# Optimization experiments

Measured on AMD Instinct MI355X. Metric: run time of the kernel, lower is better.

Reference implementation:

```python
import jax, jax.numpy as jnp
import numpy as np

COMMITMENT_COST = 0.25


def setup_inputs() -> dict:
    key = jax.random.key(0)
    k1, k2 = jax.random.split(key)
    inputs = jax.random.normal(k1, (32, 1024, 256), dtype=jnp.float32)
    codebook = jax.random.normal(k2, (8192, 256), dtype=jnp.float32)
    return {"inputs": inputs, "codebook": codebook}


def reference(inputs, codebook):
    input_shape = inputs.shape
    D = codebook.shape[1]
    K = codebook.shape[0]
    flat = inputs.reshape(-1, D)                      # [N, D]
    N = flat.shape[0]

    distances = (
        jnp.sum(flat * flat, axis=1, keepdims=True)
        + jnp.sum(codebook * codebook, axis=1)
        - 2.0 * flat @ codebook.T
    )                                                  # [N, K]
    idx = jnp.argmin(distances, axis=1)               # [N]

    # gather (equivalent to one-hot @ codebook)
    quantized = jnp.take(codebook, idx, axis=0).reshape(input_shape)

    # straight-through estimator
    quantized_st = inputs + jax.lax.stop_gradient(quantized - inputs)

    e_latent_loss = jnp.mean((jax.lax.stop_gradient(quantized_st) - inputs) ** 2)
    q_latent_loss = jnp.mean((quantized - jax.lax.stop_gradient(inputs)) ** 2)
    commitment_loss = COMMITMENT_COST * e_latent_loss
    codebook_loss = q_latent_loss
    vq_loss = commitment_loss + codebook_loss

    # perplexity of codebook usage (avg one-hot probs)
    counts = jnp.zeros((K,), dtype=inputs.dtype).at[idx].add(1.0)
    avg_probs = counts / N
    perplexity = jnp.exp(-jnp.sum(avg_probs * jnp.log(avg_probs + 1e-10)))

    tokens = idx.reshape(input_shape[:-1])
    return quantized_st, tokens, vq_loss, commitment_loss, codebook_loss, perplexity
```

## Files before the change

### kernel.cpp

```cpp
#include <hip/hip_runtime.h>
#include <stdint.h>

typedef unsigned short u16;
typedef unsigned long long u64;

#define N_ROWS 32768
#define DIM 256
#define K_CODES 8192
#define TAU 0.3f

#define A_OFF     0ull
#define B_OFF     16777216ull
#define CN_OFF    20971520ull
#define PART1_OFF 21004288ull
#define PART2_OFF 22052864ull
#define IDX_OFF   22577152ull
#define HIST_OFF  22708224ull
#define CNT_OFF   22740992ull
#define FLAG_OFF  22741008ull
#define LOSS_OFF  22872080ull
#define CBT_OFF   23068672ull
#define GMIN2_OFF 31457280ull

#define OUT_Q 0
#define OUT_T 8388608
#define OUT_S 8421376

#define BM 128
#define BN 128
#define BK 64
#define JSPLIT 4
#define RSPLIT 4

#define PACK_INF ((((u64)0xFF800000u) << 32) | 0xFFFFFFFFull)

typedef _Float16 half8 __attribute__((ext_vector_type(8)));
typedef float floatx4 __attribute__((ext_vector_type(4)));

__device__ __forceinline__ void gload_lds16(const void* g, void* l) {
    __builtin_amdgcn_global_load_lds(
        (const __attribute__((address_space(1))) void*)g,
        (__attribute__((address_space(3))) void*)l,
        16, 0, 0);
}

__device__ __forceinline__ unsigned sortable(float v) {
    unsigned u = __float_as_uint(v);
    return (u & 0x80000000u) ? ~u : (u | 0x80000000u);
}
__device__ __forceinline__ float unsortable(unsigned u) {
    return (u & 0x80000000u) ? __uint_as_float(u & 0x7fffffffu) : __uint_as_float(~u);
}
__device__ __forceinline__ u64 shfl64x(u64 v, int m) {
    return ((u64)(unsigned)__shfl_xor((int)(v >> 32), m, 64) << 32) |
           (unsigned)__shfl_xor((int)(v & 0xffffffffu), m, 64);
}
__device__ __forceinline__ u64 u64min(u64 a, u64 b) { return a < b ? a : b; }
__device__ __forceinline__ u64 u64max(u64 a, u64 b) { return a > b ? a : b; }

__global__ void prep(const float* __restrict__ inp, const float* __restrict__ cb,
                     u16* __restrict__ A, u16* __restrict__ B, float* __restrict__ cn) {
    int g = blockIdx.x * 256 + threadIdx.x;
    int row = g >> 5;
    int kc = (g & 31) << 3;
    bool isA = row < N_ROWS;
    const float* src = isA ? inp + (size_t)row * DIM + kc
                           : cb + (size_t)(row - N_ROWS) * DIM + kc;
    u16* dst = isA ? A + (size_t)row * DIM + kc
                   : B + (size_t)(row - N_ROWS) * DIM + kc;
    float4 x0 = *(const float4*)(src);
    float4 x1 = *(const float4*)(src + 4);
    float xs[8] = {x0.x, x0.y, x0.z, x0.w, x1.x, x1.y, x1.z, x1.w};
    half8 hv;
    float s = 0.f;
#pragma unroll
    for (int i = 0; i < 8; ++i) {
        hv[i] = (_Float16)xs[i];
        s = fmaf(xs[i], xs[i], s);
    }
    *(half8*)(dst) = hv;
    if (!isA) {
#pragma unroll
        for (int m = 1; m <= 16; m <<= 1) s += __shfl_xor(s, m, 64);
        if ((g & 31) == 0) cn[row - N_ROWS] = s;
    }
}

__global__ void transpose_cb(const float* __restrict__ cb, float* __restrict__ cbT) {
    __shared__ float tile[64][65];
    const int tid = threadIdx.x;
    const int tj = blockIdx.x * 64;
    const int td = blockIdx.y * 64;
    const int c = (tid & 15) * 4;
    const int r0 = tid >> 4;
#pragma unroll
    for (int p = 0; p < 4; ++p) {
        int r = p * 16 + r0;
        float4 v = *(const float4*)(cb + (size_t)(tj + r) * DIM + td + c);
        tile[r][c] = v.x; tile[r][c + 1] = v.y; tile[r][c + 2] = v.z; tile[r][c + 3] = v.w;
    }
    __syncthreads();
#pragma unroll
    for (int p = 0; p < 4; ++p) {
        int rr = p * 16 + r0;
        float4 w = {tile[c][rr], tile[c + 1][rr], tile[c + 2][rr], tile[c + 3][rr]};
        *(float4*)(cbT + (size_t)(td + rr) * K_CODES + tj + c) = w;
    }
}

__launch_bounds__(256, 2)
__global__ void vq_pass1(const u16* __restrict__ A, const u16* __restrict__ B,
                         const float* __restrict__ cn,
                         u64* __restrict__ part1, float* __restrict__ part2) {
    __shared__ __align__(16) _Float16 lsA[BM * BK];
    __shared__ __align__(16) _Float16 lsB[BN * BK];
    __shared__ u64 t1buf[BM];
    __shared__ float t2buf[BM];

    const int tid = threadIdx.x;
    const int lane = tid & 63;
    const int w = tid >> 6;
    const int wm = w >> 1, wn = w & 1;
    const int l15 = lane & 15;
    const int quad = lane >> 4;
    const int xm = l15 & 7;
    const int rowBase = blockIdx.x * BM;
    const int jBase = blockIdx.y * (K_CODES / JSPLIT);

    float d1[16], d2[16];
    unsigned idxr[16];
#pragma unroll
    for (int i = 0; i < 16; ++i) {
        d1[i] = __builtin_inff(); d2[i] = __builtin_inff(); idxr[i] = 0xffffffffu;
    }

    const int str = tid >> 3;
    const int sk16 = tid & 7;

    for (int jc = 0; jc < (K_CODES / JSPLIT) / BN; ++jc) {
        const int colBase = jBase + jc * BN;
        floatx4 acc[4][4];
#pragma unroll
        for (int mi = 0; mi < 4; ++mi)
#pragma unroll
            for (int ni = 0; ni < 4; ++ni)
                acc[mi][ni] = (floatx4){0.f, 0.f, 0.f, 0.f};

#pragma unroll 1
        for (int kk = 0; kk < DIM; kk += BK) {
#pragma unroll
            for (int it = 0; it < 4; ++it) {
                int r = it * 32 + str;
                int cdat = sk16 ^ (r & 7);
                int ch = it * 256 + tid;
                gload_lds16(A + (size_t)(rowBase + r) * DIM + kk + cdat * 8,
                            (char*)lsA + ch * 16);
                gload_lds16(B + (size_t)(colBase + r) * DIM + kk + cdat * 8,
                            (char*)lsB + ch * 16);
            }
            __syncthreads();
#pragma unroll
            for (int s = 0; s < 2; ++s) {
                const int koff = ((s * 4 + quad) ^ xm) * 8;
                half8 af[4], bf[4];
#pragma unroll
                for (int mi = 0; mi < 4; ++mi)
                    af[mi] = *(const half8*)(lsA + (wm * 64 + mi * 16 + l15) * BK + koff);
#pragma unroll
                for (int ni = 0; ni < 4; ++ni)
                    bf[ni] = *(const half8*)(lsB + (wn * 64 + ni * 16 + l15) * BK + koff);
#pragma unroll
                for (int mi = 0; mi < 4; ++mi)
#pragma unroll
                    for (int ni = 0; ni < 4; ++ni)
                        acc[mi][ni] = __builtin_amdgcn_mfma_f32_16x16x32_f16(
                            af[mi], bf[ni], acc[mi][ni], 0, 0, 0);
            }
            __syncthreads();
        }

#pragma unroll
        for (int ni = 0; ni < 4; ++ni) {
            unsigned j = (unsigned)(colBase + wn * 64 + ni * 16 + l15);
            float cnj = cn[j];
#pragma unroll
            for (int mi = 0; mi < 4; ++mi) {
#pragma unroll
                for (int r = 0; r < 4; ++r) {
                    int tr = mi * 4 + r;
                    float val = fmaf(-2.0f, acc[mi][ni][r], cnj);
                    bool lt = val < d1[tr];
                    float sec = lt ? d1[tr] : val;
                    d2[tr] = fminf(d2[tr], sec);
                    d1[tr] = lt ? val : d1[tr];
                    idxr[tr] = lt ? j : idxr[tr];
                }
            }
        }
    }

    u64 m1[16];
#pragma unroll
    for (int tr = 0; tr < 16; ++tr)
        m1[tr] = ((u64)sortable(d1[tr]) << 32) | idxr[tr];
#pragma unroll
    for (int m = 1; m <= 8; m <<= 1)
#pragma unroll
        for (int tr = 0; tr < 16; ++tr) {
            u64 o1 = shfl64x(m1[tr], m);
            float o2 = __shfl_xor(d2[tr], m, 64);
            u64 n1 = u64min(m1[tr], o1);
            float big = unsortable((unsigned)(u64max(m1[tr], o1) >> 32));
            d2[tr] = fminf(big, fminf(d2[tr], o2));
            m1[tr] = n1;
        }

    if (wn == 0 && l15 == 0) {
#pragma unroll
        for (int tr = 0; tr < 16; ++tr) {
            int rl = wm * 64 + (tr >> 2) * 16 + quad * 4 + (tr & 3);
            t1buf[rl] = m1[tr]; t2buf[rl] = d2[tr];
        }
    }
    __syncthreads();
    if (wn == 1 && l15 == 0) {
#pragma unroll
        for (int tr = 0; tr < 16; ++tr) {
            int rl = wm * 64 + (tr >> 2) * 16 + quad * 4 + (tr & 3);
            u64 o1 = t1buf[rl];
            float o2 = t2buf[rl];
            u64 n1 = u64min(m1[tr], o1);
            float big = unsortable((unsigned)(u64max(m1[tr], o1) >> 32));
            float n2 = fminf(big, fminf(d2[tr], o2));
            size_t p = (size_t)(rowBase + rl) * JSPLIT + blockIdx.y;
            part1[p] = n1;
            part2[p] = n2;
        }
    }
}

__global__ void vq_merge(const u64* __restrict__ part1, const float* __restrict__ part2,
                         unsigned* __restrict__ idx32,
                         int* __restrict__ flaglist, int* __restrict__ cnt) {
    int row = blockIdx.x * 256 + threadIdx.x;
    u64 m1 = PACK_INF;
    float f2 = __builtin_inff();
#pragma unroll
    for (int y = 0; y < JSPLIT; ++y) {
        u64 p1 = part1[(size_t)row * JSPLIT + y];
        float p2 = part2[(size_t)row * JSPLIT + y];
        u64 n1 = u64min(m1, p1);
        float big = unsortable((unsigned)(u64max(m1, p1) >> 32));
        f2 = fminf(big, fminf(f2, p2));
        m1 = n1;
    }
    idx32[row] = (unsigned)(m1 & 0xffffffffu);
    float f1 = unsortable((unsigned)(m1 >> 32));
    if (f2 - f1 < TAU) {
        int p = atomicAdd(cnt, 1);
        flaglist[p] = row;
    }
}

__global__ void vq_recompute(const float* __restrict__ inp, const float* __restrict__ cbT,
                             const float* __restrict__ cn, const int* __restrict__ flaglist,
                             const int* __restrict__ cnt, u64* __restrict__ gmin2) {
    __shared__ float xsT[DIM][8];
    __shared__ u64 wred[8][8];
    const int tid = threadIdx.x;
    const int w = tid >> 6, lane = tid & 63;
    const int n = *cnt;
    const int base = blockIdx.x * 8;
    if (base >= n) return;

    {
        int li = base + w;
        int row = flaglist[li < n ? li : (n - 1)];
        float4 a = ((const float4*)(inp + (size_t)row * DIM))[lane];
        int d0 = lane * 4;
        xsT[d0 + 0][w] = a.x; xsT[d0 + 1][w] = a.y;
        xsT[d0 + 2][w] = a.z; xsT[d0 + 3][w] = a.w;
    }
    __syncthreads();

    const int cbase = blockIdx.y * (K_CODES / RSPLIT) + tid * 4;
    float4 acc[8];
#pragma unroll
    for (int r = 0; r < 8; ++r) acc[r] = (float4){0.f, 0.f, 0.f, 0.f};

    float4 cv = *(const float4*)(cbT + cbase);
#pragma unroll 4
    for (int d = 0; d < DIM - 1; ++d) {
        float4 nx = *(const float4*)(cbT + (size_t)(d + 1) * K_CODES + cbase);
        float4 xa = *(const float4*)&xsT[d][0];
        float4 xb = *(const float4*)&xsT[d][4];
        float xv[8] = {xa.x, xa.y, xa.z, xa.w, xb.x, xb.y, xb.z, xb.w};
#pragma unroll
        for (int r = 0; r < 8; ++r) {
            acc[r].x = fmaf(xv[r], cv.x, acc[r].x);
            acc[r].y = fmaf(xv[r], cv.y, acc[r].y);
            acc[r].z = fmaf(xv[r], cv.z, acc[r].z);
            acc[r].w = fmaf(xv[r], cv.w, acc[r].w);
        }
        cv = nx;
    }
    {
        const int d = DIM - 1;
        float4 xa = *(const float4*)&xsT[d][0];
        float4 xb = *(const float4*)&xsT[d][4];
        float xv[8] = {xa.x, xa.y, xa.z, xa.w, xb.x, xb.y, xb.z, xb.w};
#pragma unroll
        for (int r = 0; r < 8; ++r) {
            acc[r].x = fmaf(xv[r], cv.x, acc[r].x);
            acc[r].y = fmaf(xv[r], cv.y, acc[r].y);
            acc[r].z = fmaf(xv[r], cv.z, acc[r].z);
            acc[r].w = fmaf(xv[r], cv.w, acc[r].w);
        }
    }

    u64 best[8];
    float4 cn4 = *(const float4*)(cn + cbase);
#pragma unroll
    for (int r = 0; r < 8; ++r) {
        float d0 = cn4.x - 2.0f * acc[r].x;
        float d1 = cn4.y - 2.0f * acc[r].y;
        float d2 = cn4.z - 2.0f * acc[r].z;
        float d3 = cn4.w - 2.0f * acc[r].w;
        u64 b = ((u64)sortable(d0) << 32) | (unsigned)(cbase + 0);
        b = u64min(b, ((u64)sortable(d1) << 32) | (unsigned)(cbase + 1));
        b = u64min(b, ((u64)sortable(d2) << 32) | (unsigned)(cbase + 2));
        b = u64min(b, ((u64)sortable(d3) << 32) | (unsigned)(cbase + 3));
        best[r] = b;
    }

#pragma unroll
    for (int m = 1; m <= 32; m <<= 1)
#pragma unroll
        for (int r = 0; r < 8; ++r) best[r] = u64min(best[r], shfl64x(best[r], m));
    if (lane < 8) wred[w][lane] = best[lane];
    __syncthreads();
    if (tid < 8 && base + tid < n) {
        u64 b = wred[0][tid];
#pragma unroll
        for (int ww = 1; ww < 8; ++ww) b = u64min(b, wred[ww][tid]);
        atomicMin(&gmin2[flaglist[base + tid]], b);
    }
}

__global__ void vq_writeback(const u64* __restrict__ gmin2, const int* __restrict__ flaglist,
                             const int* __restrict__ cnt, unsigned* __restrict__ idx32) {
    int i = blockIdx.x * 256 + threadIdx.x;
    if (i < *cnt) {
        int row = flaglist[i];
        idx32[row] = (unsigned)(gmin2[row] & 0xffffffffull);
    }
}

__global__ void vq_gather(const float* __restrict__ inp, const float* __restrict__ cb,
                          const unsigned* __restrict__ idx32, float* __restrict__ out,
                          float* __restrict__ losspart, unsigned int* __restrict__ hist) {
    __shared__ float red[4];
    int w = threadIdx.x >> 6, lane = threadIdx.x & 63;
    int i = blockIdx.x * 4 + w;
    unsigned idx = idx32[i];
    float4 c = ((const float4*)(cb + (size_t)idx * DIM))[lane];
    float4 x = ((const float4*)(inp + (size_t)i * DIM))[lane];
    ((float4*)(out + OUT_Q))[(size_t)i * 64 + lane] = c;
    float dx = c.x - x.x, dy = c.y - x.y, dz = c.z - x.z, dw = c.w - x.w;
    float s = dx * dx + dy * dy + dz * dz + dw * dw;
#pragma unroll
    for (int m = 32; m; m >>= 1) s += __shfl_xor(s, m, 64);
    if (lane == 0) {
        out[OUT_T + i] = (float)idx;
        red[w] = s;
        atomicAdd(&hist[idx], 1u);
    }
    __syncthreads();
    if (threadIdx.x == 0)
        losspart[blockIdx.x] = red[0] + red[1] + red[2] + red[3];
}

__global__ void vq_finalize(const unsigned int* __restrict__ hist,
                            const float* __restrict__ losspart, float* __restrict__ out) {
    __shared__ float redp[256], redl[256];
    int tid = threadIdx.x;
    float sp = 0.f, sl = 0.f;
    for (int k = tid; k < K_CODES; k += 256) {
        float p = (float)hist[k] * (1.0f / (float)N_ROWS);
        sp += p * logf(p + 1e-10f);
        sl += losspart[k];
    }
    redp[tid] = sp; redl[tid] = sl;
    __syncthreads();
    for (int st = 128; st; st >>= 1) {
        if (tid < st) { redp[tid] += redp[tid + st]; redl[tid] += redl[tid + st]; }
        __syncthreads();
    }
    if (tid == 0) {
        float perp = expf(-redp[0]);
        float e = redl[0] / 8388608.0f;
        out[OUT_S + 0] = 1.25f * e;
        out[OUT_S + 1] = 0.25f * e;
        out[OUT_S + 2] = e;
        out[OUT_S + 3] = perp;
    }
}

extern "C" void kernel_launch(void* const* d_in, const int* in_sizes, int n_in,
                              void* d_out, int out_size, void* d_ws, size_t ws_size,
                              hipStream_t stream) {
    const float* inp = (const float*)d_in[0];
    const float* cb = (const float*)d_in[1];
    float* out = (float*)d_out;
    char* ws = (char*)d_ws;
    u16* A = (u16*)(ws + A_OFF);
    u16* B = (u16*)(ws + B_OFF);
    float* cn = (float*)(ws + CN_OFF);
    u64* part1 = (u64*)(ws + PART1_OFF);
    float* part2 = (float*)(ws + PART2_OFF);
    unsigned* idx32 = (unsigned*)(ws + IDX_OFF);
    unsigned int* hist = (unsigned int*)(ws + HIST_OFF);
    int* cnt = (int*)(ws + CNT_OFF);
    int* flaglist = (int*)(ws + FLAG_OFF);
    float* losspart = (float*)(ws + LOSS_OFF);
    float* cbT = (float*)(ws + CBT_OFF);
    u64* gmin2 = (u64*)(ws + GMIN2_OFF);

    hipMemsetAsync(hist, 0, K_CODES * 4 + 16, stream);
    hipMemsetAsync(gmin2, 0xFF, N_ROWS * 8, stream);

    prep<<<5120, 256, 0, stream>>>(inp, cb, A, B, cn);
    transpose_cb<<<dim3(K_CODES / 64, DIM / 64), 256, 0, stream>>>(cb, cbT);
    vq_pass1<<<dim3(N_ROWS / BM, JSPLIT), 256, 0, stream>>>(A, B, cn, part1, part2);
    vq_merge<<<N_ROWS / 256, 256, 0, stream>>>(part1, part2, idx32, flaglist, cnt);
    vq_recompute<<<dim3(N_ROWS / 8, RSPLIT), 512, 0, stream>>>(inp, cbT, cn, flaglist, cnt, gmin2);
    vq_writeback<<<N_ROWS / 256, 256, 0, stream>>>(gmin2, flaglist, cnt, idx32);
    vq_gather<<<N_ROWS / 4, 256, 0, stream>>>(inp, cb, idx32, out, losspart, hist);
    vq_finalize<<<1, 256, 0, stream>>>(hist, losspart, out);
}
```

Measured before the change: 403.2 us.

## Keep A tile in registers and double-buffer codebook tiles in pass1

Measured after the change: 410.8 us. No clear change (+1.9%).

```diff
diff --git a/kernel.cpp b/kernel.cpp
--- a/kernel.cpp
+++ b/kernel.cpp
@@ -27,9 +27,9 @@
 #define OUT_S 8421376
 
 #define BM 128
-#define BN 128
-#define BK 64
+#define BNT 64
 #define JSPLIT 4
+#define NJC ((K_CODES / JSPLIT) / BNT)
 #define RSPLIT 4
 
 #define PACK_INF ((((u64)0xFF800000u) << 32) | 0xFFFFFFFFull)
@@ -108,96 +108,106 @@
     }
 }
 
-__launch_bounds__(256, 2)
+#define STAGE_B(BUFP, JCV)                                                    \
+    {                                                                         \
+        const u16* bsrc = B + (size_t)(jBase + (JCV) * BNT) * DIM;            \
+        _Pragma("unroll")                                                     \
+        for (int r_ = 0; r_ < 4; ++r_) {                                      \
+            int idx_ = r_ * 512 + tid;                                        \
+            int col_ = idx_ >> 5;                                             \
+            int sc_ = idx_ & 31;                                              \
+            int csrc_ = (sc_ & 24) | ((sc_ & 7) ^ (col_ & 7));                \
+            gload_lds16(bsrc + (size_t)col_ * DIM + csrc_ * 8,                \
+                        (char*)(BUFP) + idx_ * 16);                           \
+        }                                                                     \
+    }
+
+#define TOP2(JT, CNV)                                                         \
+    {                                                                         \
+        unsigned jj = (unsigned)(jBase + (JT) * BNT + colLoc);                \
+        _Pragma("unroll")                                                     \
+        for (int mi_ = 0; mi_ < 4; ++mi_) {                                   \
+            _Pragma("unroll")                                                 \
+            for (int r_ = 0; r_ < 4; ++r_) {                                  \
+                int tr_ = mi_ * 4 + r_;                                       \
+                float val_ = fmaf(-2.0f, acc[mi_][r_], (CNV));                \
+                float nd2_ = __builtin_amdgcn_fmed3f(d1[tr_], d2[tr_], val_); \
+                bool lt_ = val_ < d1[tr_];                                    \
+                d1[tr_] = fminf(d1[tr_], val_);                               \
+                idxr[tr_] = lt_ ? jj : idxr[tr_];                             \
+                d2[tr_] = nd2_;                                               \
+            }                                                                 \
+        }                                                                     \
+    }
+
+__launch_bounds__(512, 2)
 __global__ void vq_pass1(const u16* __restrict__ A, const u16* __restrict__ B,
                          const float* __restrict__ cn,
                          u64* __restrict__ part1, float* __restrict__ part2) {
-    __shared__ __align__(16) _Float16 lsA[BM * BK];
-    __shared__ __align__(16) _Float16 lsB[BN * BK];
-    __shared__ u64 t1buf[BM];
-    __shared__ float t2buf[BM];
+    __shared__ __align__(16) _Float16 lsB[2][BNT * DIM];
 
     const int tid = threadIdx.x;
     const int lane = tid & 63;
     const int w = tid >> 6;
-    const int wm = w >> 1, wn = w & 1;
+    const int wm = w >> 2;
+    const int wn = w & 3;
     const int l15 = lane & 15;
     const int quad = lane >> 4;
     const int xm = l15 & 7;
+    const int colLoc = wn * 16 + l15;
     const int rowBase = blockIdx.x * BM;
     const int jBase = blockIdx.y * (K_CODES / JSPLIT);
 
+    STAGE_B(lsB[0], 0);
+    float cn_c = cn[jBase + colLoc];
+
+    half8 af[4][8];
+    {
+        const u16* aRow = A + (size_t)(rowBase + wm * 64 + l15) * DIM + quad * 8;
+#pragma unroll
+        for (int mi = 0; mi < 4; ++mi)
+#pragma unroll
+            for (int ks = 0; ks < 8; ++ks)
+                af[mi][ks] = *(const half8*)(aRow + (size_t)mi * 16 * DIM + ks * 32);
+    }
+
     float d1[16], d2[16];
     unsigned idxr[16];
 #pragma unroll
     for (int i = 0; i < 16; ++i) {
         d1[i] = __builtin_inff(); d2[i] = __builtin_inff(); idxr[i] = 0xffffffffu;
     }
-
-    const int str = tid >> 3;
-    const int sk16 = tid & 7;
-
-    for (int jc = 0; jc < (K_CODES / JSPLIT) / BN; ++jc) {
-        const int colBase = jBase + jc * BN;
-        floatx4 acc[4][4];
-#pragma unroll
-        for (int mi = 0; mi < 4; ++mi)
-#pragma unroll
-            for (int ni = 0; ni < 4; ++ni)
-                acc[mi][ni] = (floatx4){0.f, 0.f, 0.f, 0.f};
+    floatx4 acc[4];
+    float cn_p = 0.f, cn_n = 0.f;
 
 #pragma unroll 1
-        for (int kk = 0; kk < DIM; kk += BK) {
-#pragma unroll
-            for (int it = 0; it < 4; ++it) {
-                int r = it * 32 + str;
-                int cdat = sk16 ^ (r & 7);
-                int ch = it * 256 + tid;
-                gload_lds16(A + (size_t)(rowBase + r) * DIM + kk + cdat * 8,
-                            (char*)lsA + ch * 16);
-                gload_lds16(B + (size_t)(colBase + r) * DIM + kk + cdat * 8,
-                            (char*)lsB + ch * 16);
-            }
-            __syncthreads();
-#pragma unroll
-            for (int s = 0; s < 2; ++s) {
-                const int koff = ((s * 4 + quad) ^ xm) * 8;
-                half8 af[4], bf[4];
-#pragma unroll
-                for (int mi = 0; mi < 4; ++mi)
-                    af[mi] = *(const half8*)(lsA + (wm * 64 + mi * 16 + l15) * BK + koff);
-#pragma unroll
-                for (int ni = 0; ni < 4; ++ni)
-                    bf[ni] = *(const half8*)(lsB + (wn * 64 + ni * 16 + l15) * BK + koff);
-#pragma unroll
-                for (int mi = 0; mi < 4; ++mi)
-#pragma unroll
-                    for (int ni = 0; ni < 4; ++ni)
-                        acc[mi][ni] = __builtin_amdgcn_mfma_f32_16x16x32_f16(
-                            af[mi], bf[ni], acc[mi][ni], 0, 0, 0);
-            }
-            __syncthreads();
-        }
-
-#pragma unroll
-        for (int ni = 0; ni < 4; ++ni) {
-            unsigned j = (unsigned)(colBase + wn * 64 + ni * 16 + l15);
-            float cnj = cn[j];
-#pragma unroll
-            for (int mi = 0; mi < 4; ++mi) {
-#pragma unroll
-                for (int r = 0; r < 4; ++r) {
-                    int tr = mi * 4 + r;
-                    float val = fmaf(-2.0f, acc[mi][ni][r], cnj);
-                    bool lt = val < d1[tr];
-                    float sec = lt ? d1[tr] : val;
-                    d2[tr] = fminf(d2[tr], sec);
-                    d1[tr] = lt ? val : d1[tr];
-                    idxr[tr] = lt ? j : idxr[tr];
-                }
-            }
-        }
-    }
+    for (int jc = 0; jc < NJC; ++jc) {
+        if (jc < NJC - 1) {
+            STAGE_B(lsB[(jc + 1) & 1], jc + 1);
+            cn_n = cn[jBase + (jc + 1) * BNT + colLoc];
+        }
+        if (jc > 0) TOP2(jc - 1, cn_p);
+        if (jc < NJC - 1) asm volatile("s_waitcnt vmcnt(5)" ::: "memory");
+        else              asm volatile("s_waitcnt vmcnt(0)" ::: "memory");
+        __builtin_amdgcn_s_barrier();
+
+        const _Float16* bcur = lsB[jc & 1];
+#pragma unroll
+        for (int mi = 0; mi < 4; ++mi) acc[mi] = (floatx4){0.f, 0.f, 0.f, 0.f};
+#pragma unroll
+        for (int ks = 0; ks < 8; ++ks) {
+            const int c = ks * 4 + quad;
+            const int scw = (c & 24) | ((c & 7) ^ xm);
+            half8 bfv = *(const half8*)((const char*)bcur + colLoc * 512 + scw * 16);
+#pragma unroll
+            for (int mi = 0; mi < 4; ++mi)
+                acc[mi] = __builtin_amdgcn_mfma_f32_16x16x32_f16(
+                    af[mi][ks], bfv, acc[mi], 0, 0, 0);
+        }
+        __builtin_amdgcn_s_barrier();
+        cn_p = cn_c; cn_c = cn_n;
+    }
+    TOP2(NJC - 1, cn_p);
 
     u64 m1[16];
 #pragma unroll
@@ -215,27 +225,33 @@
             m1[tr] = n1;
         }
 
-    if (wn == 0 && l15 == 0) {
+    u64* t1 = (u64*)lsB[0];
+    float* t2 = (float*)((char*)lsB[0] + 4 * BM * 8);
+    __syncthreads();
+    if (l15 == 0) {
 #pragma unroll
         for (int tr = 0; tr < 16; ++tr) {
             int rl = wm * 64 + (tr >> 2) * 16 + quad * 4 + (tr & 3);
-            t1buf[rl] = m1[tr]; t2buf[rl] = d2[tr];
-        }
-    }
-    __syncthreads();
-    if (wn == 1 && l15 == 0) {
-#pragma unroll
-        for (int tr = 0; tr < 16; ++tr) {
-            int rl = wm * 64 + (tr >> 2) * 16 + quad * 4 + (tr & 3);
-            u64 o1 = t1buf[rl];
-            float o2 = t2buf[rl];
-            u64 n1 = u64min(m1[tr], o1);
-            float big = unsortable((unsigned)(u64max(m1[tr], o1) >> 32));
-            float n2 = fminf(big, fminf(d2[tr], o2));
-            size_t p = (size_t)(rowBase + rl) * JSPLIT + blockIdx.y;
-            part1[p] = n1;
-            part2[p] = n2;
-        }
+            t1[wn * BM + rl] = m1[tr];
+            t2[wn * BM + rl] = d2[tr];
+        }
+    }
+    __syncthreads();
+    if (tid < BM) {
+        u64 b1 = t1[tid];
+        float b2 = t2[tid];
+#pragma unroll
+        for (int y = 1; y < 4; ++y) {
+            u64 o1 = t1[y * BM + tid];
+            float o2 = t2[y * BM + tid];
+            u64 n1 = u64min(b1, o1);
+            float big = unsortable((unsigned)(u64max(b1, o1) >> 32));
+            b2 = fminf(big, fminf(b2, o2));
+            b1 = n1;
+        }
+        size_t p = (size_t)(rowBase + tid) * JSPLIT + blockIdx.y;
+        part1[p] = b1;
+        part2[p] = b2;
     }
 }
 
@@ -431,7 +447,7 @@
 
     prep<<<5120, 256, 0, stream>>>(inp, cb, A, B, cn);
     transpose_cb<<<dim3(K_CODES / 64, DIM / 64), 256, 0, stream>>>(cb, cbT);
-    vq_pass1<<<dim3(N_ROWS / BM, JSPLIT), 256, 0, stream>>>(A, B, cn, part1, part2);
+    vq_pass1<<<dim3(N_ROWS / BM, JSPLIT), 512, 0, stream>>>(A, B, cn, part1, part2);
     vq_merge<<<N_ROWS / 256, 256, 0, stream>>>(part1, part2, idx32, flaglist, cnt);
     vq_recompute<<<dim3(N_ROWS / 8, RSPLIT), 512, 0, stream>>>(inp, cbT, cn, flaglist, cnt, gmin2);
     vq_writeback<<<N_ROWS / 256, 256, 0, stream>>>(gmin2, flaglist, cnt, idx32);
```

## Double-buffer LDS tiles in pass1 GEMM and fold memsets into kernels

Applied to the files above, without the earlier changes.

Result: faster. 391.6 us (-2.9%).

```diff
diff --git a/kernel.cpp b/kernel.cpp
--- a/kernel.cpp
+++ b/kernel.cpp
@@ -30,6 +30,7 @@
 #define BN 128
 #define BK 64
 #define JSPLIT 4
+#define NT (4 * ((K_CODES / JSPLIT) / BN))
 #define RSPLIT 4
 
 #define PACK_INF ((((u64)0xFF800000u) << 32) | 0xFFFFFFFFull)
@@ -59,7 +60,14 @@
 __device__ __forceinline__ u64 u64max(u64 a, u64 b) { return a > b ? a : b; }
 
 __global__ void prep(const float* __restrict__ inp, const float* __restrict__ cb,
-                     u16* __restrict__ A, u16* __restrict__ B, float* __restrict__ cn) {
+                     u16* __restrict__ A, u16* __restrict__ B, float* __restrict__ cn,
+                     unsigned int* __restrict__ hist, int* __restrict__ cnt) {
+    if (blockIdx.x >= 5120) {
+        int i = (blockIdx.x - 5120) * 256 + threadIdx.x;
+        if (i < K_CODES) hist[i] = 0u;
+        else if (i < K_CODES + 4) cnt[i - K_CODES] = 0;
+        return;
+    }
     int g = blockIdx.x * 256 + threadIdx.x;
     int row = g >> 5;
     int kc = (g & 31) << 3;
@@ -108,12 +116,29 @@
     }
 }
 
+#define STAGE_T(T, BUFI)                                                      \
+    {                                                                         \
+        const int jc_ = (T) >> 2;                                             \
+        const int kk_ = ((T) & 3) * BK;                                       \
+        const int colBase_ = jBase + jc_ * BN;                                \
+        _Pragma("unroll")                                                     \
+        for (int it_ = 0; it_ < 4; ++it_) {                                   \
+            int r_ = it_ * 32 + str;                                          \
+            int cdat_ = sk16 ^ (r_ & 7);                                      \
+            int ch_ = it_ * 256 + tid;                                        \
+            gload_lds16(A + (size_t)(rowBase + r_) * DIM + kk_ + cdat_ * 8,   \
+                        (char*)lsA[BUFI] + ch_ * 16);                         \
+            gload_lds16(B + (size_t)(colBase_ + r_) * DIM + kk_ + cdat_ * 8,  \
+                        (char*)lsB[BUFI] + ch_ * 16);                         \
+        }                                                                     \
+    }
+
 __launch_bounds__(256, 2)
 __global__ void vq_pass1(const u16* __restrict__ A, const u16* __restrict__ B,
                          const float* __restrict__ cn,
                          u64* __restrict__ part1, float* __restrict__ part2) {
-    __shared__ __align__(16) _Float16 lsA[BM * BK];
-    __shared__ __align__(16) _Float16 lsB[BN * BK];
+    __shared__ __align__(16) _Float16 lsA[2][BM * BK];
+    __shared__ __align__(16) _Float16 lsB[2][BN * BK];
     __shared__ u64 t1buf[BM];
     __shared__ float t2buf[BM];
 
@@ -137,66 +162,70 @@
     const int str = tid >> 3;
     const int sk16 = tid & 7;
 
-    for (int jc = 0; jc < (K_CODES / JSPLIT) / BN; ++jc) {
-        const int colBase = jBase + jc * BN;
-        floatx4 acc[4][4];
-#pragma unroll
-        for (int mi = 0; mi < 4; ++mi)
+    STAGE_T(0, 0);
+    asm volatile("s_waitcnt vmcnt(0)" ::: "memory");
+    __builtin_amdgcn_s_barrier();
+    asm volatile("" ::: "memory");
+
+    floatx4 acc[4][4];
+    int buf = 0;
+
+#pragma unroll 1
+    for (int t = 0; t < NT; ++t) {
+        if (t + 1 < NT) STAGE_T(t + 1, buf ^ 1);
+
+        if ((t & 3) == 0) {
+#pragma unroll
+            for (int mi = 0; mi < 4; ++mi)
+#pragma unroll
+                for (int ni = 0; ni < 4; ++ni)
+                    acc[mi][ni] = (floatx4){0.f, 0.f, 0.f, 0.f};
+        }
+
+#pragma unroll
+        for (int s = 0; s < 2; ++s) {
+            const int koff = ((s * 4 + quad) ^ xm) * 8;
+            half8 af[4], bf[4];
+#pragma unroll
+            for (int mi = 0; mi < 4; ++mi)
+                af[mi] = *(const half8*)(lsA[buf] + (wm * 64 + mi * 16 + l15) * BK + koff);
 #pragma unroll
             for (int ni = 0; ni < 4; ++ni)
-                acc[mi][ni] = (floatx4){0.f, 0.f, 0.f, 0.f};
-
-#pragma unroll 1
-        for (int kk = 0; kk < DIM; kk += BK) {
-#pragma unroll
-            for (int it = 0; it < 4; ++it) {
-                int r = it * 32 + str;
-                int cdat = sk16 ^ (r & 7);
-                int ch = it * 256 + tid;
-                gload_lds16(A + (size_t)(rowBase + r) * DIM + kk + cdat * 8,
-                            (char*)lsA + ch * 16);
-                gload_lds16(B + (size_t)(colBase + r) * DIM + kk + cdat * 8,
-                            (char*)lsB + ch * 16);
-            }
-            __syncthreads();
-#pragma unroll
-            for (int s = 0; s < 2; ++s) {
-                const int koff = ((s * 4 + quad) ^ xm) * 8;
-                half8 af[4], bf[4];
-#pragma unroll
-                for (int mi = 0; mi < 4; ++mi)
-                    af[mi] = *(const half8*)(lsA + (wm * 64 + mi * 16 + l15) * BK + koff);
+                bf[ni] = *(const half8*)(lsB[buf] + (wn * 64 + ni * 16 + l15) * BK + koff);
+#pragma unroll
+            for (int mi = 0; mi < 4; ++mi)
 #pragma unroll
                 for (int ni = 0; ni < 4; ++ni)
-                    bf[ni] = *(const half8*)(lsB + (wn * 64 + ni * 16 + l15) * BK + koff);
-#pragma unroll
-                for (int mi = 0; mi < 4; ++mi)
-#pragma unroll
-                    for (int ni = 0; ni < 4; ++ni)
-                        acc[mi][ni] = __builtin_amdgcn_mfma_f32_16x16x32_f16(
-                            af[mi], bf[ni], acc[mi][ni], 0, 0, 0);
-            }
-            __syncthreads();
-        }
-
-#pragma unroll
-        for (int ni = 0; ni < 4; ++ni) {
-            unsigned j = (unsigned)(colBase + wn * 64 + ni * 16 + l15);
-            float cnj = cn[j];
-#pragma unroll
-            for (int mi = 0; mi < 4; ++mi) {
-#pragma unroll
-                for (int r = 0; r < 4; ++r) {
-                    int tr = mi * 4 + r;
-                    float val = fmaf(-2.0f, acc[mi][ni][r], cnj);
-                    bool lt = val < d1[tr];
-                    float sec = lt ? d1[tr] : val;
-                    d2[tr] = fminf(d2[tr], sec);
-                    d1[tr] = lt ? val : d1[tr];
-                    idxr[tr] = lt ? j : idxr[tr];
+                    acc[mi][ni] = __builtin_amdgcn_mfma_f32_16x16x32_f16(
+                        af[mi], bf[ni], acc[mi][ni], 0, 0, 0);
+        }
+
+        if ((t & 3) == 3) {
+            const int colBase = jBase + (t >> 2) * BN;
+#pragma unroll
+            for (int ni = 0; ni < 4; ++ni) {
+                unsigned j = (unsigned)(colBase + wn * 64 + ni * 16 + l15);
+                float cnj = cn[j];
+#pragma unroll
+                for (int mi = 0; mi < 4; ++mi) {
+#pragma unroll
+                    for (int r = 0; r < 4; ++r) {
+                        int tr = mi * 4 + r;
+                        float val = fmaf(-2.0f, acc[mi][ni][r], cnj);
+                        bool lt = val < d1[tr];
+                        float sec = lt ? d1[tr] : val;
+                        d2[tr] = fminf(d2[tr], sec);
+                        d1[tr] = lt ? val : d1[tr];
+                        idxr[tr] = lt ? j : idxr[tr];
+                    }
                 }
             }
         }
+
+        asm volatile("s_waitcnt vmcnt(0)" ::: "memory");
+        __builtin_amdgcn_s_barrier();
+        asm volatile("" ::: "memory");
+        buf ^= 1;
     }
 
     u64 m1[16];
@@ -241,7 +270,8 @@
 
 __global__ void vq_merge(const u64* __restrict__ part1, const float* __restrict__ part2,
                          unsigned* __restrict__ idx32,
-                         int* __restrict__ flaglist, int* __restrict__ cnt) {
+                         int* __restrict__ flaglist, int* __restrict__ cnt,
+                         u64* __restrict__ gmin2) {
     int row = blockIdx.x * 256 + threadIdx.x;
     u64 m1 = PACK_INF;
     float f2 = __builtin_inff();
@@ -254,6 +284,7 @@
         f2 = fminf(big, fminf(f2, p2));
         m1 = n1;
     }
+    gmin2[row] = PACK_INF;
     idx32[row] = (unsigned)(m1 & 0xffffffffu);
     float f1 = unsortable((unsigned)(m1 >> 32));
     if (f2 - f1 < TAU) {
@@ -426,13 +457,10 @@
     float* cbT = (float*)(ws + CBT_OFF);
     u64* gmin2 = (u64*)(ws + GMIN2_OFF);
 
-    hipMemsetAsync(hist, 0, K_CODES * 4 + 16, stream);
-    hipMemsetAsync(gmin2, 0xFF, N_ROWS * 8, stream);
-
-    prep<<<5120, 256, 0, stream>>>(inp, cb, A, B, cn);
+    prep<<<5153, 256, 0, stream>>>(inp, cb, A, B, cn, hist, cnt);
     transpose_cb<<<dim3(K_CODES / 64, DIM / 64), 256, 0, stream>>>(cb, cbT);
     vq_pass1<<<dim3(N_ROWS / BM, JSPLIT), 256, 0, stream>>>(A, B, cn, part1, part2);
-    vq_merge<<<N_ROWS / 256, 256, 0, stream>>>(part1, part2, idx32, flaglist, cnt);
+    vq_merge<<<N_ROWS / 256, 256, 0, stream>>>(part1, part2, idx32, flaglist, cnt, gmin2);
     vq_recompute<<<dim3(N_ROWS / 8, RSPLIT), 512, 0, stream>>>(inp, cbT, cn, flaglist, cnt, gmin2);
     vq_writeback<<<N_ROWS / 256, 256, 0, stream>>>(gmin2, flaglist, cnt, idx32);
     vq_gather<<<N_ROWS / 4, 256, 0, stream>>>(inp, cb, idx32, out, losspart, hist);
```
